# Optimization experiments

Hardware: AMD Instinct MI355X
Metric: run time of the kernel (lower is better)

The kernel has to match this reference:

```python
import jax, jax.numpy as jnp
import numpy as np

S, P = 4, 6  # states, stack-encoding depth; detector has S*9**P rows


def _build_cd(s, p):
    """Vectorized construction of ConfigurationDetector1's weight/bias.

    Each of the 9**p multi-indices i = (i_top[0..p-1], i_nonempty[0..p-1]) is
    encoded by p base-9 digits: digit 0 -> (None, None); digit d in 1..8 ->
    symbol v=(d-1)//2 in {0..3} with top present iff (d-1)%2==1.
    convert_to_tensor_indices maps position j (of 2p) value a to column a+4j,
    so i_top occupies cols [0,4p) and i_nonempty cols [4p,8p).
    """
    N9 = 9 ** p
    powers = 9 ** np.arange(p - 1, -1, -1)
    digits = (np.arange(N9)[:, None] // powers) % 9        # (N9, p)
    nonzero = digits > 0
    v = np.where(nonzero, (digits - 1) // 2, 0)            # symbol in {0..3}
    has_top = nonzero & (((digits - 1) % 2) == 1)
    k = nonzero.sum(1) + has_top.sum(1)                    # nnz count per i

    Wi = np.zeros((N9, 8 * p), np.float32)
    rows = np.broadcast_to(np.arange(N9)[:, None], (N9, p))
    col_ne = 4 * p + 4 * np.arange(p) + v                  # nonempty columns
    Wi[rows[nonzero], col_ne[nonzero]] = 1.0
    col_top = 4 * np.arange(p) + v                         # top columns
    Wi[rows[has_top], col_top[has_top]] = 1.0

    R = s * N9                                             # row = i_idx*s + z
    W = np.zeros((R, 8 * p + s), np.float32)
    W[:, :8 * p] = np.repeat(Wi, s, axis=0)
    K = np.repeat(k, s)
    z = np.tile(np.arange(s), N9)
    W[np.arange(R), 8 * p + z] = np.where(K == 0, 1.0, K * (4 * p + 2)).astype(np.float32)
    b = np.where(K == 0, 0.0, -(K * (4 * p + 2)).astype(np.float64)).astype(np.float32)
    return W, b


def _small_linears(p):
    q = 10.0 * p * p
    w_stack = np.zeros((p, 4 * p), np.float32)
    for kk in range(p):
        w_stack[kk, 4 * kk:4 * kk + 4] = 1.0
    w_nss = np.zeros((4 * p, p), np.float32)
    b_nss = np.zeros(4 * p, np.float32)
    w_nst = np.zeros((4 * p, p), np.float32)
    for i in range(p):
        w_nss[4 * i + 0, i] = 1.0
        b_nss[4 * i + 0] = 0.0
        w_nss[4 * i + 1, i] = 1.0 / q
        b_nss[4 * i + 1] = (q - 4 * p - 1) / q
        w_nss[4 * i + 2, i] = 1.0 / q
        b_nss[4 * i + 2] = (q - 1) / q
        w_nss[4 * i + 3, i] = q
        b_nss[4 * i + 3] = -q + 4 * p + 1
        w_nst[4 * i + 3, i] = -4.0
    w_st = ((2 * p + 1) * q * np.eye(4 * p)).astype(np.float32)
    b_st = (-(2 * p + 1) * (q - 2.0) * np.ones(4 * p)).astype(np.float32)
    w_sn = (q * np.eye(4 * p)).astype(np.float32)
    b_sn = (-(q - 4 * p - 2.0) * np.ones(4 * p)).astype(np.float32)
    return w_stack, w_nss, b_nss, w_nst, w_st, b_st, w_sn, b_sn


def setup_inputs() -> dict:
    s, p = S, P
    key = jax.random.key(0)
    kx, kb, kg = jax.random.split(key, 3)
    W, b = _build_cd(s, p)
    R = s * 9 ** p
    bound = 1.0 / np.sqrt(R)  # torch Linear default init bound (fan_in = R)
    beta_w = jax.random.uniform(kb, (s, R), jnp.float32, -bound, bound)
    gamma_w = jax.random.uniform(kg, (4 * p, R), jnp.float32, -bound, bound)
    x = jax.random.normal(kx, (s + 12 * p,), jnp.float32)
    w_stack, w_nss, b_nss, w_nst, w_st, b_st, w_sn, b_sn = _small_linears(p)
    return {
        "x": x,
        "cd_w": jnp.asarray(W), "cd_b": jnp.asarray(b),
        "beta_w": beta_w, "gamma_w": gamma_w,
        "w_stack": jnp.asarray(w_stack),
        "w_nss": jnp.asarray(w_nss), "b_nss": jnp.asarray(b_nss),
        "w_nst": jnp.asarray(w_nst),
        "w_st": jnp.asarray(w_st), "b_st": jnp.asarray(b_st),
        "w_sn": jnp.asarray(w_sn), "b_sn": jnp.asarray(b_sn),
    }


def _sat(v):
    # saturated_relu: sigma(x) = min(max(x, 0), 1)
    return jnp.clip(v, 0.0, 1.0)


def reference(x, cd_w, cd_b, beta_w, gamma_w, w_stack, w_nss, b_nss,
              w_nst, w_st, b_st, w_sn, b_sn):
    s, p = S, P
    state = x[:s]
    noisy_sub_stack = x[s:s + 4 * p]
    noisy_sub_top = x[s + 4 * p:s + 8 * p]
    noisy_sub_nonempty = x[s + 8 * p:]

    w_in = jnp.concatenate([noisy_sub_top, noisy_sub_nonempty, state])  # (8p+s,)
    cd_out = _sat(cd_w @ w_in + cd_b)                                   # (s*9^p,)

    stack = w_stack @ _sat(noisy_sub_stack)                             # (p,)
    top = w_stack @ _sat(noisy_sub_top)                                 # (p,) linear_top is linear_stack

    next_state = beta_w @ cd_out                                        # (s,)
    next_noisy_sub_stack = (w_nss @ stack + b_nss) + (w_nst @ top) + (gamma_w @ cd_out) - 1.0
    next_noisy_sub_top = w_st @ next_noisy_sub_stack + b_st
    next_noisy_sub_nonempty = w_sn @ next_noisy_sub_stack + b_sn
    return jnp.concatenate([next_state, next_noisy_sub_stack,
                            next_noisy_sub_top, next_noisy_sub_nonempty])
```

## Files before the change

kernel.cpp:

```cpp
#include <hip/hip_runtime.h>


#define PN9    531441
#define CHUNKS 64
#define TPB    256

__device__ __forceinline__ float satf(float v) {
    return fminf(fmaxf(v, 0.0f), 1.0f);
}

__global__ __launch_bounds__(TPB) void ss_main(
    const float* __restrict__ x,
    const float* __restrict__ beta_w,
    const float* __restrict__ gamma_w,
    float* __restrict__ partials)
{
    __shared__ float2 tab2[243];
    __shared__ float st[4];
    __shared__ float red[TPB / 64];

    const int t = threadIdx.x;
    if (t < 243) {
        const int jj = t / 81, d2 = t % 81;
        const int da = d2 / 9;
        const int db = d2 % 9;
        float S = 0.0f, K = 0.0f;
        if (da > 0) {
            const int v = (da - 1) >> 1, ht = (da - 1) & 1, j = 2 * jj;
            S += x[52 + 4 * j + v] + (ht ? x[28 + 4 * j + v] : 0.0f);
            K += (float)(1 + ht);
        }
        if (db > 0) {
            const int v = (db - 1) >> 1, ht = (db - 1) & 1, j = 2 * jj + 1;
            S += x[52 + 4 * j + v] + (ht ? x[28 + 4 * j + v] : 0.0f);
            K += (float)(1 + ht);
        }
        float2 e; e.x = S; e.y = K;
        tab2[t] = e;
    }
    if (t >= 248 && t < 252) st[t - 248] = x[t - 248];
    __syncthreads();

    const float s0 = st[0], s1 = st[1], s2 = st[2], s3 = st[3];

    const int u = blockIdx.y;
    const float4* __restrict__ row =
        (u < 4) ? ((const float4*)beta_w  + (size_t)u * PN9)
                : ((const float4*)gamma_w + (size_t)(u - 4) * PN9);

    auto body = [&](int i, const float4 v) -> float {
        unsigned tmp = (unsigned)i;
        float S = 0.0f, K = 0.0f;
#pragma unroll
        for (int jj = 2; jj >= 0; --jj) {
            const unsigned d2 = tmp % 81u;
            tmp /= 81u;
            const float2 e = tab2[jj * 81 + d2];
            S += e.x;
            K += e.y;
        }
        const float km = 26.0f * K;
        const bool  k0 = (K == 0.0f);
        const float c  = k0 ? 1.0f : km;
        const float base = S - (k0 ? 0.0f : km);
        return v.x * satf(base + c * s0)
             + v.y * satf(base + c * s1)
             + v.z * satf(base + c * s2)
             + v.w * satf(base + c * s3);
    };

    const int stride = CHUNKS * TPB;
    float a0 = 0.0f, a1 = 0.0f, a2 = 0.0f, a3 = 0.0f;

    int i = blockIdx.x * TPB + t;
    for (; i + 3 * stride < PN9; i += 4 * stride) {
        const float4 v0 = row[i];
        const float4 v1 = row[i + stride];
        const float4 v2 = row[i + 2 * stride];
        const float4 v3 = row[i + 3 * stride];
        a0 += body(i,              v0);
        a1 += body(i + stride,     v1);
        a2 += body(i + 2 * stride, v2);
        a3 += body(i + 3 * stride, v3);
    }
    for (; i < PN9; i += stride) a0 += body(i, row[i]);

    float acc = (a0 + a1) + (a2 + a3);

#pragma unroll
    for (int off = 32; off > 0; off >>= 1) acc += __shfl_down(acc, off, 64);
    const int wave = t >> 6, lane = t & 63;
    if (lane == 0) red[wave] = acc;
    __syncthreads();
    if (t == 0)
        partials[(size_t)u * CHUNKS + blockIdx.x] =
            red[0] + red[1] + red[2] + red[3];
}

__global__ __launch_bounds__(256) void ss_epi(
    const float* __restrict__ x,
    const float* __restrict__ w_stack,
    const float* __restrict__ w_nss, const float* __restrict__ b_nss,
    const float* __restrict__ w_nst,
    const float* __restrict__ w_st,  const float* __restrict__ b_st,
    const float* __restrict__ w_sn,  const float* __restrict__ b_sn,
    const float* __restrict__ partials,
    float* __restrict__ out)
{
    __shared__ float sums[28];
    __shared__ float stk[6], top[6], nns[24];

    const int t = threadIdx.x;

    if (t < 224) {
        const int u = t >> 3, g = t & 7;
        float v = 0.0f;
#pragma unroll
        for (int c = 0; c < 8; ++c) v += partials[(size_t)u * CHUNKS + g * 8 + c];
#pragma unroll
        for (int off = 4; off > 0; off >>= 1) v += __shfl_down(v, off, 8);
        if (g == 0) sums[u] = v;
    }
    if (t >= 224 && t < 230) {
        const int k = t - 224;
        float v = 0.0f;
        for (int c = 0; c < 24; ++c) v += w_stack[k * 24 + c] * satf(x[4 + c]);
        stk[k] = v;
    }
    if (t >= 230 && t < 236) {
        const int k = t - 230;
        float v = 0.0f;
        for (int c = 0; c < 24; ++c) v += w_stack[k * 24 + c] * satf(x[28 + c]);
        top[k] = v;
    }
    __syncthreads();

    if (t < 24) {
        float v = b_nss[t] + sums[4 + t] - 1.0f;
        for (int c = 0; c < 6; ++c)
            v += w_nss[t * 6 + c] * stk[c] + w_nst[t * 6 + c] * top[c];
        nns[t] = v;
    }
    __syncthreads();

    if (t < 4) {
        out[t] = sums[t];
    } else if (t < 28) {
        out[t] = nns[t - 4];
    } else if (t < 52) {
        const int r = t - 28;
        float v = b_st[r];
        for (int c = 0; c < 24; ++c) v += w_st[r * 24 + c] * nns[c];
        out[t] = v;
    } else if (t < 76) {
        const int r = t - 52;
        float v = b_sn[r];
        for (int c = 0; c < 24; ++c) v += w_sn[r * 24 + c] * nns[c];
        out[t] = v;
    }
}

extern "C" void kernel_launch(void* const* d_in, const int* in_sizes, int n_in,
                              void* d_out, int out_size, void* d_ws, size_t ws_size,
                              hipStream_t stream) {
    const float* x       = (const float*)d_in[0];
    const float* beta_w  = (const float*)d_in[3];
    const float* gamma_w = (const float*)d_in[4];
    const float* w_stack = (const float*)d_in[5];
    const float* w_nss   = (const float*)d_in[6];
    const float* b_nss   = (const float*)d_in[7];
    const float* w_nst   = (const float*)d_in[8];
    const float* w_st    = (const float*)d_in[9];
    const float* b_st    = (const float*)d_in[10];
    const float* w_sn    = (const float*)d_in[11];
    const float* b_sn    = (const float*)d_in[12];

    float* partials = (float*)d_ws;
    float* out      = (float*)d_out;

    dim3 grid(CHUNKS, 28);
    ss_main<<<grid, TPB, 0, stream>>>(x, beta_w, gamma_w, partials);
    ss_epi<<<1, 256, 0, stream>>>(x, w_stack, w_nss, b_nss, w_nst,
                                  w_st, b_st, w_sn, b_sn, partials, out);
}
```

Measured before the change: 46.47 us.

## Fuse epilogue into main kernel via last-block atomic ticket; nontemporal weight loads

The separate epilogue kernel is folded into the main streaming kernel. Each block writes its partial sum and takes an atomic ticket, and the last block to finish does the final reduction and the small matrix-vector products, then resets the counter. This removes a second kernel launch and the gap between launches. Weight loads also switch to nontemporal loads because the large weight matrices are read once. The cost is one atomic per block and a reliance on the workspace counter being zeroed before the first call.

```diff
diff --git a/kernel.cpp b/kernel.cpp
--- a/kernel.cpp
+++ b/kernel.cpp
@@ -4,20 +4,32 @@
 #define PN9    531441
 #define CHUNKS 64
 #define TPB    256
+#define NROWS  28
+#define TOTAL_BLOCKS (CHUNKS * NROWS)
+
+typedef float vf4 __attribute__((ext_vector_type(4)));
 
 __device__ __forceinline__ float satf(float v) {
     return fminf(fmaxf(v, 0.0f), 1.0f);
 }
 
-__global__ __launch_bounds__(TPB) void ss_main(
+__global__ __launch_bounds__(TPB) void ss_fused(
     const float* __restrict__ x,
     const float* __restrict__ beta_w,
     const float* __restrict__ gamma_w,
-    float* __restrict__ partials)
+    const float* __restrict__ w_stack,
+    const float* __restrict__ w_nss, const float* __restrict__ b_nss,
+    const float* __restrict__ w_nst,
+    const float* __restrict__ w_st,  const float* __restrict__ b_st,
+    const float* __restrict__ w_sn,  const float* __restrict__ b_sn,
+    float* __restrict__ partials,
+    unsigned int* __restrict__ counter,
+    float* __restrict__ out)
 {
     __shared__ float2 tab2[243];
     __shared__ float st[4];
     __shared__ float red[TPB / 64];
+    __shared__ unsigned int sticket;
 
     const int t = threadIdx.x;
     if (t < 243) {
@@ -44,11 +56,11 @@
     const float s0 = st[0], s1 = st[1], s2 = st[2], s3 = st[3];
 
     const int u = blockIdx.y;
-    const float4* __restrict__ row =
-        (u < 4) ? ((const float4*)beta_w  + (size_t)u * PN9)
-                : ((const float4*)gamma_w + (size_t)(u - 4) * PN9);
+    const vf4* __restrict__ row =
+        (u < 4) ? ((const vf4*)beta_w  + (size_t)u * PN9)
+                : ((const vf4*)gamma_w + (size_t)(u - 4) * PN9);
 
-    auto body = [&](int i, const float4 v) -> float {
+    auto body = [&](int i, const vf4 v) -> float {
         unsigned tmp = (unsigned)i;
         float S = 0.0f, K = 0.0f;
 #pragma unroll
@@ -74,16 +86,16 @@
 
     int i = blockIdx.x * TPB + t;
     for (; i + 3 * stride < PN9; i += 4 * stride) {
-        const float4 v0 = row[i];
-        const float4 v1 = row[i + stride];
-        const float4 v2 = row[i + 2 * stride];
-        const float4 v3 = row[i + 3 * stride];
+        const vf4 v0 = __builtin_nontemporal_load(&row[i]);
+        const vf4 v1 = __builtin_nontemporal_load(&row[i + stride]);
+        const vf4 v2 = __builtin_nontemporal_load(&row[i + 2 * stride]);
+        const vf4 v3 = __builtin_nontemporal_load(&row[i + 3 * stride]);
         a0 += body(i,              v0);
         a1 += body(i + stride,     v1);
         a2 += body(i + 2 * stride, v2);
         a3 += body(i + 3 * stride, v3);
     }
-    for (; i < PN9; i += stride) a0 += body(i, row[i]);
+    for (; i < PN9; i += stride) a0 += body(i, __builtin_nontemporal_load(&row[i]));
 
     float acc = (a0 + a1) + (a2 + a3);
 
@@ -92,34 +104,27 @@
     const int wave = t >> 6, lane = t & 63;
     if (lane == 0) red[wave] = acc;
     __syncthreads();
-    if (t == 0)
+    if (t == 0) {
         partials[(size_t)u * CHUNKS + blockIdx.x] =
             red[0] + red[1] + red[2] + red[3];
-}
+        sticket = __hip_atomic_fetch_add(counter, 1u, __ATOMIC_ACQ_REL,
+                                         __HIP_MEMORY_SCOPE_AGENT);
+    }
+    __syncthreads();
 
-__global__ __launch_bounds__(256) void ss_epi(
-    const float* __restrict__ x,
-    const float* __restrict__ w_stack,
-    const float* __restrict__ w_nss, const float* __restrict__ b_nss,
-    const float* __restrict__ w_nst,
-    const float* __restrict__ w_st,  const float* __restrict__ b_st,
-    const float* __restrict__ w_sn,  const float* __restrict__ b_sn,
-    const float* __restrict__ partials,
-    float* __restrict__ out)
-{
+    if (sticket % TOTAL_BLOCKS != TOTAL_BLOCKS - 1) return;
+
     __shared__ float sums[28];
     __shared__ float stk[6], top[6], nns[24];
 
-    const int t = threadIdx.x;
-
     if (t < 224) {
-        const int u = t >> 3, g = t & 7;
+        const int uu = t >> 3, g = t & 7;
         float v = 0.0f;
 #pragma unroll
-        for (int c = 0; c < 8; ++c) v += partials[(size_t)u * CHUNKS + g * 8 + c];
+        for (int c = 0; c < 8; ++c) v += partials[(size_t)uu * CHUNKS + g * 8 + c];
 #pragma unroll
         for (int off = 4; off > 0; off >>= 1) v += __shfl_down(v, off, 8);
-        if (g == 0) sums[u] = v;
+        if (g == 0) sums[uu] = v;
     }
     if (t >= 224 && t < 230) {
         const int k = t - 224;
@@ -158,6 +163,9 @@
         for (int c = 0; c < 24; ++c) v += w_sn[r * 24 + c] * nns[c];
         out[t] = v;
     }
+
+    if (t == 0)
+        __hip_atomic_store(counter, 0u, __ATOMIC_RELEASE, __HIP_MEMORY_SCOPE_AGENT);
 }
 
 extern "C" void kernel_launch(void* const* d_in, const int* in_sizes, int n_in,
@@ -175,11 +183,13 @@
     const float* w_sn    = (const float*)d_in[11];
     const float* b_sn    = (const float*)d_in[12];
 
-    float* partials = (float*)d_ws;
-    float* out      = (float*)d_out;
+    float*        partials = (float*)d_ws;
+    unsigned int* counter  = (unsigned int*)((char*)d_ws + NROWS * CHUNKS * 4);
+    float*        out      = (float*)d_out;
 
-    dim3 grid(CHUNKS, 28);
-    ss_main<<<grid, TPB, 0, stream>>>(x, beta_w, gamma_w, partials);
-    ss_epi<<<1, 256, 0, stream>>>(x, w_stack, w_nss, b_nss, w_nst,
-                                  w_st, b_st, w_sn, b_sn, partials, out);
+    dim3 grid(CHUNKS, NROWS);
+    ss_fused<<<grid, TPB, 0, stream>>>(x, beta_w, gamma_w,
+                                       w_stack, w_nss, b_nss, w_nst,
+                                       w_st, b_st, w_sn, b_sn,
+                                       partials, counter, out);
 }
```

New measurement: 130.6 us. 2.81x slower.
